# Optimization experiments

Measured on AMD Instinct MI355X. Metric: run time of the kernel, lower is better.

The kernel has to match this reference:

```python
import jax, jax.numpy as jnp
import numpy as np

B, T, E = 4, 2048, 1024
NUM_HEADS = 16
HEAD_SIZE = E // NUM_HEADS


def _rope_tables(T, E):
    # thetas over pairs, repeat_interleave by 2 -> shape (E,)
    thetas = 10000.0 ** (-jnp.arange(0, E, 2, dtype=jnp.float32) / E)
    thetas = jnp.repeat(thetas, 2)
    angles = jnp.arange(T, dtype=jnp.float32)[:, None] * thetas[None, :]  # (T, E)
    return jnp.sin(angles), jnp.cos(angles)


def _rotate(x, sin, cos):
    # x: (B, T, E); pairs (x0, x1) -> (-x1, x0)
    Bx, Tx, Ex = x.shape
    xp = x.reshape(Bx, Tx, Ex // 2, 2)
    rot = jnp.stack([-xp[..., 1], xp[..., 0]], axis=-1).reshape(Bx, Tx, Ex)
    return x * cos + rot * sin


def setup_inputs() -> dict:
    key = jax.random.key(0)
    ks = jax.random.split(key, 6)
    scale = 1.0 / np.sqrt(E)
    return {
        "input": jax.random.normal(ks[0], (B, T, E), dtype=jnp.float32),
        "Wq": jax.random.normal(ks[1], (E, E), dtype=jnp.float32) * scale,
        "Wk": jax.random.normal(ks[2], (E, E), dtype=jnp.float32) * scale,
        "Wv": jax.random.normal(ks[3], (E, E), dtype=jnp.float32) * scale,
        "Wo": jax.random.normal(ks[4], (E, E), dtype=jnp.float32) * scale,
        "bo": jnp.zeros((E,), dtype=jnp.float32),
    }


def reference(input, Wq, Wk, Wv, Wo, bo):
    Bx, Tx, Ex = input.shape
    sin, cos = _rope_tables(Tx, Ex)
    rx = _rotate(input, sin, cos)
    q = rx @ Wq.T
    k = rx @ Wk.T
    v = input @ Wv.T
    # (B, H, T, hd)
    def split_heads(t):
        return t.reshape(Bx, Tx, NUM_HEADS, HEAD_SIZE).transpose(0, 2, 1, 3)
    q, k, v = split_heads(q), split_heads(k), split_heads(v)
    scores = jnp.einsum("bhqd,bhkd->bhqk", q, k)
    causal = jnp.tril(jnp.ones((Tx, Tx), dtype=bool))
    scores = jnp.where(causal[None, None], scores, -jnp.inf) / np.sqrt(HEAD_SIZE)
    attn = jax.nn.softmax(scores, axis=-1)  # dropout omitted (eval mode)
    out = jnp.einsum("bhqk,bhkd->bhqd", attn, v)
    out = out.transpose(0, 2, 1, 3).reshape(Bx, Tx, Ex)
    return out @ Wo.T + bo
```

## Files before the change

### kernel.cpp

```cpp
#include <hip/hip_runtime.h>

typedef unsigned short u16;
typedef unsigned int   u32;
typedef __attribute__((ext_vector_type(4))) float f32x4;
typedef __attribute__((ext_vector_type(8))) __bf16 bf16x8;
typedef __attribute__((ext_vector_type(2))) u32  u32x2;
typedef __attribute__((ext_vector_type(4))) u32  u32x4;

#define LDS_CAST(p) ((__attribute__((address_space(3))) void*)(p))
#define GLB_CAST(p) ((const __attribute__((address_space(1))) void*)(p))

__device__ __forceinline__ void load_lds16(const void* g, void* l) {
    __builtin_amdgcn_global_load_lds(GLB_CAST(g), LDS_CAST(l), 16, 0, 0);
}

__device__ __forceinline__ u32 lds_off(const void* p) {
    return (u32)(size_t)(const __attribute__((address_space(3))) void*)p;
}

__device__ __forceinline__ u16 f2bf(float f) {
    union { float f; u32 u; } v; v.f = f;
    u32 r = (v.u + 0x7FFFu + ((v.u >> 16) & 1u)) >> 16;
    return (u16)r;
}

__device__ __forceinline__ u16 bfc(float f) {
    return __builtin_bit_cast(u16, (__bf16)f);
}
__device__ __forceinline__ u32 pack_bf16(float a, float b) {
    return (u32)bfc(a) | ((u32)bfc(b) << 16);
}

__device__ __forceinline__ float exp2fast(float x) {
#if __has_builtin(__builtin_amdgcn_exp2f)
    return __builtin_amdgcn_exp2f(x);
#else
    return __expf(x * 0.6931471805599453f);
#endif
}

__global__ __launch_bounds__(256) void rope_cast(const float* __restrict__ x,
                                                 u16* __restrict__ xb,
                                                 u16* __restrict__ rxb) {
    int idx = blockIdx.x * 256 + threadIdx.x;
    int e2 = (idx & 511) * 2;
    int t  = (idx >> 9) & 2047;
    float2 v = *(const float2*)&x[(size_t)idx * 2];
    float theta = expf(-0.0089944730194981f * (float)e2);
    float angle = (float)t * theta;
    float sa, ca;
    sincosf(angle, &sa, &ca);
    float r0 = v.x * ca - v.y * sa;
    float r1 = v.y * ca + v.x * sa;
    u32 xp  = (u32)f2bf(v.x) | ((u32)f2bf(v.y) << 16);
    u32 rxp = (u32)f2bf(r0)  | ((u32)f2bf(r1)  << 16);
    *(u32*)&xb[(size_t)idx * 2]  = xp;
    *(u32*)&rxb[(size_t)idx * 2] = rxp;
}

__global__ __launch_bounds__(256) void wcast(const float* __restrict__ a,
                                             const float* __restrict__ b,
                                             const float* __restrict__ c,
                                             const float* __restrict__ d,
                                             u16* __restrict__ out) {
    int i = blockIdx.x * 256 + threadIdx.x;
    int w = i >> 20, j = i & 1048575;
    float v = (w == 0) ? a[j] : (w == 1) ? b[j] : (w == 2) ? c[j] : d[j];
    out[i] = f2bf(v);
}

template <int MODE>
__global__ __launch_bounds__(256) void gemm128(const u16* __restrict__ A0,
                                               const u16* __restrict__ A1,
                                               const u16* __restrict__ W,
                                               u16* __restrict__ outb,
                                               float* __restrict__ outf,
                                               const float* __restrict__ bias) {
    constexpr int Kd = 1024;
    __shared__ u16 As[128 * 64];
    __shared__ u16 Bs[128 * 64];
    const int tid = threadIdx.x;
    const int m0 = blockIdx.x * 128;
    const int n0 = blockIdx.y * 128;
    const u16* A = (MODE == 0 && n0 >= 2048) ? A1 : A0;
    const int wid = tid >> 6, lane = tid & 63;
    const int wr = wid >> 1, wc = wid & 1;
    const int lr = lane & 15, lhi = lane >> 4;

    f32x4 acc[4][4] = {};

    for (int k0 = 0; k0 < Kd; k0 += 64) {
        if (k0) __syncthreads();
#pragma unroll
        for (int i = 0; i < 4; ++i) {
            int cidx = tid + 256 * i;
            int row = cidx >> 3, col = (cidx & 7) * 8;
            load_lds16(A + (size_t)(m0 + row) * Kd + k0 + col, &As[row * 64 + col]);
        }
#pragma unroll
        for (int i = 0; i < 4; ++i) {
            int cidx = tid + 256 * i;
            int row = cidx >> 3, col = (cidx & 7) * 8;
            load_lds16(W + (size_t)(n0 + row) * Kd + k0 + col, &Bs[row * 64 + col]);
        }
        __syncthreads();
#pragma unroll
        for (int c = 0; c < 2; ++c) {
            bf16x8 a[4], b[4];
#pragma unroll
            for (int m = 0; m < 4; ++m)
                a[m] = *(const bf16x8*)&As[(wr * 64 + m * 16 + lr) * 64 + c * 32 + lhi * 8];
#pragma unroll
            for (int n = 0; n < 4; ++n)
                b[n] = *(const bf16x8*)&Bs[(wc * 64 + n * 16 + lr) * 64 + c * 32 + lhi * 8];
#pragma unroll
            for (int m = 0; m < 4; ++m)
#pragma unroll
                for (int n = 0; n < 4; ++n)
                    acc[m][n] = __builtin_amdgcn_mfma_f32_16x16x32_bf16(a[m], b[n], acc[m][n], 0, 0, 0);
        }
    }

#pragma unroll
    for (int m = 0; m < 4; ++m) {
        int rowb = m0 + wr * 64 + m * 16 + lhi * 4;
#pragma unroll
        for (int n = 0; n < 4; ++n) {
            int col = n0 + wc * 64 + n * 16 + lr;
#pragma unroll
            for (int r = 0; r < 4; ++r) {
                int mg = rowb + r;
                float v = acc[m][n][r];
                if (MODE == 0) {
                    int bb = mg >> 11, t = mg & 2047;
                    int hg = col >> 6, d = col & 63;
                    outb[(size_t)(hg >> 4) * 8388608 +
                         (((size_t)(bb * 16 + (hg & 15)) * 2048) + t) * 64 + d] = bfc(v);
                } else {
                    outf[(size_t)mg * 1024 + col] = v + bias[col];
                }
            }
        }
    }
}

__device__ __forceinline__ void attn_pass(const bf16x8 (&qa)[2], f32x4 (&acc)[4],
                                          float (&m_i)[4], float (&l_i)[4],
                                          const u16* ks, const u16* vcur, u32 vsb,
                                          u16* pw, u32 ptb, int lr, int lhi,
                                          int kv0, int q0w, bool diag, bool use_tr) {
    f32x4 s4[4] = {};
    __builtin_amdgcn_s_setprio(1);
#pragma unroll
    for (int c = 0; c < 2; ++c)
#pragma unroll
        for (int n = 0; n < 4; ++n) {
            int r = n * 16 + lr;
            bf16x8 kb = *(const bf16x8*)&ks[r * 64 + ((c * 32 + lhi * 8) ^ ((r & 7) * 8))];
            s4[n] = __builtin_amdgcn_mfma_f32_16x16x32_bf16(qa[c], kb, s4[n], 0, 0, 0);
        }
    __builtin_amdgcn_s_setprio(0);

    if (diag) {
#pragma unroll
        for (int n = 0; n < 4; ++n) {
            int kvg = kv0 + n * 16 + lr;
#pragma unroll
            for (int r = 0; r < 4; ++r)
                if (kvg > q0w + lhi * 4 + r) s4[n][r] = -1e30f;
        }
    }

    float mx[4] = { -1e30f, -1e30f, -1e30f, -1e30f };
#pragma unroll
    for (int n = 0; n < 4; ++n)
#pragma unroll
        for (int r = 0; r < 4; ++r) mx[r] = fmaxf(mx[r], s4[n][r]);
#pragma unroll
    for (int off = 8; off; off >>= 1)
#pragma unroll
        for (int r = 0; r < 4; ++r) mx[r] = fmaxf(mx[r], __shfl_xor(mx[r], off));

#pragma unroll
    for (int r = 0; r < 4; ++r) {
        float mnew = fmaxf(m_i[r], mx[r]);
        float sc = exp2fast(m_i[r] - mnew);
        m_i[r] = mnew;
        l_i[r] *= sc;
#pragma unroll
        for (int nd = 0; nd < 4; ++nd) acc[nd][r] *= sc;
    }
    float rs[4] = { 0.f, 0.f, 0.f, 0.f };
#pragma unroll
    for (int n = 0; n < 4; ++n) {
        float p0 = exp2fast(s4[n][0] - m_i[0]);
        float p1 = exp2fast(s4[n][1] - m_i[1]);
        float p2 = exp2fast(s4[n][2] - m_i[2]);
        float p3 = exp2fast(s4[n][3] - m_i[3]);
        rs[0] += p0; rs[1] += p1; rs[2] += p2; rs[3] += p3;
        u32x2 wv; wv.x = pack_bf16(p0, p1); wv.y = pack_bf16(p2, p3);
        *(u32x2*)&pw[(n * 16 + lr) * 16 + lhi * 4] = wv;
    }
#pragma unroll
    for (int off = 8; off; off >>= 1)
#pragma unroll
        for (int r = 0; r < 4; ++r) rs[r] += __shfl_xor(rs[r], off);
#pragma unroll
    for (int r = 0; r < 4; ++r) l_i[r] += rs[r];

    asm volatile("s_waitcnt lgkmcnt(0)" ::: "memory");

    __builtin_amdgcn_s_setprio(1);
#pragma unroll
    for (int c = 0; c < 2; ++c) {
        union { bf16x8 v; u32 w[4]; u16 h[8]; } pa;
        union { bf16x8 v; u32 w[4]; u16 h[8]; } vb[4];
        if (use_tr) {
            u32x2 plo, phi;
            u32 paddr = ptb + (u32)(c * 1024 + lhi * 256 + lr * 2);
            asm volatile("ds_read_b64_tr_b16 %0, %2\n\t"
                         "ds_read_b64_tr_b16 %1, %2 offset:128"
                         : "=&v"(plo), "=&v"(phi) : "v"(paddr));
            u32x2 lo[4], hi[4];
#pragma unroll
            for (int nd = 0; nd < 4; ++nd) {
                u32 a = vsb + (u32)((c * 32 + lhi * 8 + nd) * 128 + lr * 2);
                asm volatile("ds_read_b64_tr_b16 %0, %2\n\t"
                             "ds_read_b64_tr_b16 %1, %2 offset:512"
                             : "=&v"(lo[nd]), "=&v"(hi[nd]) : "v"(a));
            }
            asm volatile("s_waitcnt lgkmcnt(0)" ::: "memory");
            __builtin_amdgcn_sched_barrier(0);
            pa.w[0] = plo.x; pa.w[1] = plo.y; pa.w[2] = phi.x; pa.w[3] = phi.y;
#pragma unroll
            for (int nd = 0; nd < 4; ++nd) {
                vb[nd].w[0] = lo[nd].x; vb[nd].w[1] = lo[nd].y;
                vb[nd].w[2] = hi[nd].x; vb[nd].w[3] = hi[nd].y;
            }
        } else {
#pragma unroll
            for (int i = 0; i < 8; ++i) {
                int k = c * 32 + lhi * 8 + i;
                pa.h[i] = pw[k * 16 + lr];
#pragma unroll
                for (int nd = 0; nd < 4; ++nd)
                    vb[nd].h[i] = vcur[((k >> 2) << 8) + (nd << 6) + ((k & 3) << 4) + lr];
            }
        }
#pragma unroll
        for (int nd = 0; nd < 4; ++nd)
            acc[nd] = __builtin_amdgcn_mfma_f32_16x16x32_bf16(pa.v, vb[nd].v, acc[nd], 0, 0, 0);
    }
    __builtin_amdgcn_s_setprio(0);
}

__global__ __launch_bounds__(256) void attn64(const u16* __restrict__ Q,
                                              const u16* __restrict__ K,
                                              const u16* __restrict__ V,
                                              u16* __restrict__ O) {
    constexpr int T = 2048;
    __shared__ u16 Ks[2][64 * 64];
    __shared__ u16 Vs[2][64 * 64];
    __shared__ u16 Ps[4][64 * 16];
    const int tid = threadIdx.x, wid = tid >> 6, lane = tid & 63;
    const int lr = lane & 15, lhi = lane >> 4;
    const int bh = blockIdx.y;
    const int qtA = blockIdx.x;
    const int qtB = 31 - qtA;
    const int q0wA = qtA * 64 + wid * 16;
    const int q0wB = qtB * 64 + wid * 16;
    const size_t base = (size_t)bh * T * 64;
    const u16* Qp = Q + base;
    const u16* Kp = K + base;
    const u16* Vp = V + base;

    const float QS = 0.18033688011112042f;
    bf16x8 qaA[2], qaB[2];
#pragma unroll
    for (int c = 0; c < 2; ++c) {
        bf16x8 tA = *(const bf16x8*)&Qp[(size_t)(q0wA + lr) * 64 + c * 32 + lhi * 8];
        bf16x8 tB = *(const bf16x8*)&Qp[(size_t)(q0wB + lr) * 64 + c * 32 + lhi * 8];
        bf16x8 oA, oB;
#pragma unroll
        for (int i = 0; i < 8; ++i) {
            oA[i] = (__bf16)((float)tA[i] * QS);
            oB[i] = (__bf16)((float)tB[i] * QS);
        }
        qaA[c] = oA; qaB[c] = oB;
    }

    f32x4 accA[4] = {}, accB[4] = {};
    float m_iA[4], l_iA[4], m_iB[4], l_iB[4];
#pragma unroll
    for (int r = 0; r < 4; ++r) {
        m_iA[r] = -1e30f; l_iA[r] = 0.f;
        m_iB[r] = -1e30f; l_iB[r] = 0.f;
    }

    {
        u16* vt = (u16*)&Vs[0][0];
#pragma unroll
        for (int j = 0; j < 16; ++j) vt[tid * 16 + j] = (u16)(tid * 16 + j);
    }
    __syncthreads();
    bool use_tr;
    {
        const u32 vsb0 = lds_off(&Vs[0][0]);
        bool ok = true;
#pragma unroll
        for (int t = 0; t < 2; ++t) {
            const int c = t ? 1 : 0, nd = t ? 3 : 0;
            u32 a = vsb0 + (u32)((c * 32 + lhi * 8 + nd) * 128 + lr * 2);
            u32x2 lo, hi;
            asm volatile("ds_read_b64_tr_b16 %0, %2\n\t"
                         "ds_read_b64_tr_b16 %1, %2 offset:512"
                         : "=&v"(lo), "=&v"(hi) : "v"(a));
            asm volatile("s_waitcnt lgkmcnt(0)" ::: "memory");
            __builtin_amdgcn_sched_barrier(0);
            union { u32 w[4]; u16 h[8]; } u;
            u.w[0] = lo.x; u.w[1] = lo.y; u.w[2] = hi.x; u.w[3] = hi.y;
#pragma unroll
            for (int i = 0; i < 8; ++i) {
                int k = c * 32 + lhi * 8 + i;
                int e = ((k >> 2) << 8) + (nd << 6) + ((k & 3) << 4) + lr;
                ok = ok && (u.h[i] == (u16)e);
            }
        }
        use_tr = (bool)__all((int)ok);
    }
    __syncthreads();

#define STAGE(bb, kv0s)                                                          \
    {                                                                            \
        _Pragma("unroll")                                                        \
        for (int i = 0; i < 2; ++i) {                                            \
            int q = tid + 256 * i;                                               \
            int krow = q >> 3;                                                   \
            int kcol = ((q & 7) ^ (krow & 7)) * 8;                               \
            load_lds16(Kp + (size_t)((kv0s) + krow) * 64 + kcol, &Ks[bb][q * 8]);\
            int vk = ((q >> 5) << 2) + ((q >> 1) & 3);                           \
            int vd = (((q >> 3) & 3) << 4) + ((q & 1) << 3);                     \
            load_lds16(Vp + (size_t)((kv0s) + vk) * 64 + vd, &Vs[bb][q * 8]);    \
        }                                                                        \
    }

    STAGE(0, 0);
    __syncthreads();

    u16* pw = Ps[wid];
    const u32 ptb = lds_off(pw);
    int buf = 0;
    for (int kt = 0; kt <= qtB; ++kt) {
        const int kv0 = kt * 64;
        if (kt < qtB) STAGE(buf ^ 1, kv0 + 64);

        const u16* ks = Ks[buf];
        const u16* vcur = Vs[buf];
        const u32 vsb = lds_off(vcur);

        if (kt <= qtA)
            attn_pass(qaA, accA, m_iA, l_iA, ks, vcur, vsb, pw, ptb, lr, lhi,
                      kv0, q0wA, kt == qtA, use_tr);
        attn_pass(qaB, accB, m_iB, l_iB, ks, vcur, vsb, pw, ptb, lr, lhi,
                  kv0, q0wB, kt == qtB, use_tr);

        __syncthreads();
        buf ^= 1;
    }
#undef STAGE

    const int b = bh >> 4, h = bh & 15;
#pragma unroll
    for (int nd = 0; nd < 4; ++nd)
#pragma unroll
        for (int r = 0; r < 4; ++r) {
            int d = h * 64 + nd * 16 + lr;
            int qgA = q0wA + lhi * 4 + r;
            int qgB = q0wB + lhi * 4 + r;
            O[(size_t)(b * 2048 + qgA) * 1024 + d] = bfc(accA[nd][r] / l_iA[r]);
            O[(size_t)(b * 2048 + qgB) * 1024 + d] = bfc(accB[nd][r] / l_iB[r]);
        }
}

extern "C" void kernel_launch(void* const* d_in, const int* in_sizes, int n_in,
                              void* d_out, int out_size, void* d_ws, size_t ws_size,
                              hipStream_t stream) {
    const float* x  = (const float*)d_in[0];
    const float* Wq = (const float*)d_in[1];
    const float* Wk = (const float*)d_in[2];
    const float* Wv = (const float*)d_in[3];
    const float* Wo = (const float*)d_in[4];
    const float* bo = (const float*)d_in[5];

    char* ws = (char*)d_ws;
    u16* Wqb = (u16*)ws;
    u16* Wob = Wqb + 3 * (1 << 20);
    u16* xb  = (u16*)(ws + (size_t)8 * 1024 * 1024);
    u16* rxb = xb  + (size_t)8388608;
    u16* Qb  = rxb + (size_t)8388608;
    u16* Kb  = Qb  + (size_t)8388608;
    u16* Vb  = Kb  + (size_t)8388608;
    u16* Ob  = Vb  + (size_t)8388608;

    rope_cast<<<16384, 256, 0, stream>>>(x, xb, rxb);
    wcast<<<16384, 256, 0, stream>>>(Wq, Wk, Wv, Wo, Wqb);

    gemm128<0><<<dim3(64, 24), 256, 0, stream>>>(rxb, xb, Wqb, Qb, nullptr, nullptr);

    attn64<<<dim3(16, 64), 256, 0, stream>>>(Qb, Kb, Vb, Ob);

    gemm128<1><<<dim3(64, 8), 256, 0, stream>>>(Ob, Ob, Wob, nullptr, (float*)d_out, bo);
}
```

Baseline: 372.8 us.

## Skip online-softmax rescale unless max grows; store P row-major with swizzle

The attention inner pass now rescales the accumulators and running sum only when some row's new max exceeds the stored max by more than 8 (in log2 units), checked wave-wide with __any. Otherwise it keeps the stale max, which lets P values grow up to 2^8 while staying safe in bf16 and fp32. The P tile layout changes to query-row-major with an XOR swizzle. It is written with per-element u16 stores and read back as one 128-bit vector load instead of two ds_read_b64_tr_b16 transposed reads. This trades fewer exp/multiply ops and fewer read instructions for more, smaller LDS store instructions.

```diff
diff --git a/kernel.cpp b/kernel.cpp
--- a/kernel.cpp
+++ b/kernel.cpp
@@ -26,9 +26,6 @@
 
 __device__ __forceinline__ u16 bfc(float f) {
     return __builtin_bit_cast(u16, (__bf16)f);
-}
-__device__ __forceinline__ u32 pack_bf16(float a, float b) {
-    return (u32)bfc(a) | ((u32)bfc(b) << 16);
 }
 
 __device__ __forceinline__ float exp2fast(float x) {
@@ -147,7 +144,7 @@
 __device__ __forceinline__ void attn_pass(const bf16x8 (&qa)[2], f32x4 (&acc)[4],
                                           float (&m_i)[4], float (&l_i)[4],
                                           const u16* ks, const u16* vcur, u32 vsb,
-                                          u16* pw, u32 ptb, int lr, int lhi,
+                                          u16* pw, int lr, int lhi,
                                           int kv0, int q0w, bool diag, bool use_tr) {
     f32x4 s4[4] = {};
     __builtin_amdgcn_s_setprio(1);
@@ -181,26 +178,31 @@
 #pragma unroll
         for (int r = 0; r < 4; ++r) mx[r] = fmaxf(mx[r], __shfl_xor(mx[r], off));
 
-#pragma unroll
-    for (int r = 0; r < 4; ++r) {
-        float mnew = fmaxf(m_i[r], mx[r]);
-        float sc = exp2fast(m_i[r] - mnew);
-        m_i[r] = mnew;
-        l_i[r] *= sc;
-#pragma unroll
-        for (int nd = 0; nd < 4; ++nd) acc[nd][r] *= sc;
-    }
+    bool up = false;
+#pragma unroll
+    for (int r = 0; r < 4; ++r) up = up || (mx[r] > m_i[r] + 8.0f);
+    if (__any((int)up)) {
+#pragma unroll
+        for (int r = 0; r < 4; ++r) {
+            float mnew = fmaxf(m_i[r], mx[r]);
+            float sc = exp2fast(m_i[r] - mnew);
+            m_i[r] = mnew;
+            l_i[r] *= sc;
+#pragma unroll
+            for (int nd = 0; nd < 4; ++nd) acc[nd][r] *= sc;
+        }
+    }
+
     float rs[4] = { 0.f, 0.f, 0.f, 0.f };
 #pragma unroll
-    for (int n = 0; n < 4; ++n) {
-        float p0 = exp2fast(s4[n][0] - m_i[0]);
-        float p1 = exp2fast(s4[n][1] - m_i[1]);
-        float p2 = exp2fast(s4[n][2] - m_i[2]);
-        float p3 = exp2fast(s4[n][3] - m_i[3]);
-        rs[0] += p0; rs[1] += p1; rs[2] += p2; rs[3] += p3;
-        u32x2 wv; wv.x = pack_bf16(p0, p1); wv.y = pack_bf16(p2, p3);
-        *(u32x2*)&pw[(n * 16 + lr) * 16 + lhi * 4] = wv;
-    }
+    for (int n = 0; n < 4; ++n)
+#pragma unroll
+        for (int r = 0; r < 4; ++r) {
+            float pv = exp2fast(s4[n][r] - m_i[r]);
+            rs[r] += pv;
+            int qloc = lhi * 4 + r;
+            pw[qloc * 64 + ((n * 16 + lr) ^ ((qloc & 7) * 8))] = bfc(pv);
+        }
 #pragma unroll
     for (int off = 8; off; off >>= 1)
 #pragma unroll
@@ -208,19 +210,12 @@
 #pragma unroll
     for (int r = 0; r < 4; ++r) l_i[r] += rs[r];
 
-    asm volatile("s_waitcnt lgkmcnt(0)" ::: "memory");
-
     __builtin_amdgcn_s_setprio(1);
 #pragma unroll
     for (int c = 0; c < 2; ++c) {
-        union { bf16x8 v; u32 w[4]; u16 h[8]; } pa;
+        bf16x8 pa = *(const bf16x8*)&pw[lr * 64 + ((c * 32 + lhi * 8) ^ ((lr & 7) * 8))];
         union { bf16x8 v; u32 w[4]; u16 h[8]; } vb[4];
         if (use_tr) {
-            u32x2 plo, phi;
-            u32 paddr = ptb + (u32)(c * 1024 + lhi * 256 + lr * 2);
-            asm volatile("ds_read_b64_tr_b16 %0, %2\n\t"
-                         "ds_read_b64_tr_b16 %1, %2 offset:128"
-                         : "=&v"(plo), "=&v"(phi) : "v"(paddr));
             u32x2 lo[4], hi[4];
 #pragma unroll
             for (int nd = 0; nd < 4; ++nd) {
@@ -231,7 +226,6 @@
             }
             asm volatile("s_waitcnt lgkmcnt(0)" ::: "memory");
             __builtin_amdgcn_sched_barrier(0);
-            pa.w[0] = plo.x; pa.w[1] = plo.y; pa.w[2] = phi.x; pa.w[3] = phi.y;
 #pragma unroll
             for (int nd = 0; nd < 4; ++nd) {
                 vb[nd].w[0] = lo[nd].x; vb[nd].w[1] = lo[nd].y;
@@ -239,17 +233,16 @@
             }
         } else {
 #pragma unroll
-            for (int i = 0; i < 8; ++i) {
-                int k = c * 32 + lhi * 8 + i;
-                pa.h[i] = pw[k * 16 + lr];
-#pragma unroll
-                for (int nd = 0; nd < 4; ++nd)
+            for (int nd = 0; nd < 4; ++nd)
+#pragma unroll
+                for (int i = 0; i < 8; ++i) {
+                    int k = c * 32 + lhi * 8 + i;
                     vb[nd].h[i] = vcur[((k >> 2) << 8) + (nd << 6) + ((k & 3) << 4) + lr];
-            }
+                }
         }
 #pragma unroll
         for (int nd = 0; nd < 4; ++nd)
-            acc[nd] = __builtin_amdgcn_mfma_f32_16x16x32_bf16(pa.v, vb[nd].v, acc[nd], 0, 0, 0);
+            acc[nd] = __builtin_amdgcn_mfma_f32_16x16x32_bf16(pa, vb[nd].v, acc[nd], 0, 0, 0);
     }
     __builtin_amdgcn_s_setprio(0);
 }
@@ -261,7 +254,7 @@
     constexpr int T = 2048;
     __shared__ u16 Ks[2][64 * 64];
     __shared__ u16 Vs[2][64 * 64];
-    __shared__ u16 Ps[4][64 * 16];
+    __shared__ u16 Ps[4][16 * 64];
     const int tid = threadIdx.x, wid = tid >> 6, lane = tid & 63;
     const int lr = lane & 15, lhi = lane >> 4;
     const int bh = blockIdx.y;
@@ -348,7 +341,6 @@
     __syncthreads();
 
     u16* pw = Ps[wid];
-    const u32 ptb = lds_off(pw);
     int buf = 0;
     for (int kt = 0; kt <= qtB; ++kt) {
         const int kv0 = kt * 64;
@@ -359,9 +351,9 @@
         const u32 vsb = lds_off(vcur);
 
         if (kt <= qtA)
-            attn_pass(qaA, accA, m_iA, l_iA, ks, vcur, vsb, pw, ptb, lr, lhi,
+            attn_pass(qaA, accA, m_iA, l_iA, ks, vcur, vsb, pw, lr, lhi,
                       kv0, q0wA, kt == qtA, use_tr);
-        attn_pass(qaB, accB, m_iB, l_iB, ks, vcur, vsb, pw, ptb, lr, lhi,
+        attn_pass(qaB, accB, m_iB, l_iB, ks, vcur, vsb, pw, lr, lhi,
                   kv0, q0wB, kt == qtB, use_tr);
 
         __syncthreads();
```

Measured after the change: 363.8 us. -2.4%, faster.
